# Optimization experiments

Hardware: AMD Instinct MI355X
Metric: run time of the kernel (lower is better)

## Reference

```python
import jax, jax.numpy as jnp
import numpy as np
from jax import lax

WS = (4, 8, 8)        # window_size (D,H,W)
DIM = 128
HEADS = 4
HD = DIM // HEADS      # 32
SCALE = HD ** -0.5     # swinv1, lif neuron -> head_dim**-0.5
TAU = 2.0
VTH = 1.0
ALPHA = 2.0            # ATan surrogate width


def _rel_pos_index(ws):
    # static numpy computation of relative_position_index, shape (N, N)
    coords = np.stack(np.meshgrid(np.arange(ws[0]), np.arange(ws[1]), np.arange(ws[2]), indexing='ij'))
    cf = coords.reshape(3, -1)                      # (3, N)
    rel = (cf[:, :, None] - cf[:, None, :]).transpose(1, 2, 0).astype(np.int64)  # (N,N,3)
    rel[:, :, 0] += ws[0] - 1
    rel[:, :, 1] += ws[1] - 1
    rel[:, :, 2] += ws[2] - 1
    rel[:, :, 0] *= (2 * ws[1] - 1) * (2 * ws[2] - 1)
    rel[:, :, 1] *= 2 * ws[2] - 1
    return rel.sum(-1)

RPI = _rel_pos_index(WS)  # (N, N) int


@jax.custom_vjp
def spike(x):
    return (x >= 0.0).astype(x.dtype)

def _spike_fwd(x):
    return spike(x), x

def _spike_bwd(x, g):
    # ATan surrogate gradient (spikingjelly default)
    return (g * (ALPHA / (2.0 * (1.0 + (np.pi / 2.0 * ALPHA * x) ** 2))),)

spike.defvjp(_spike_fwd, _spike_bwd)


def lif(x):
    # multi-step LIF over leading time axis: v' = v + (x - v)/tau, hard reset to 0
    def step(v, xt):
        v = v + (xt - v) / TAU
        s = spike(v - VTH)
        return v * (1.0 - s), s
    return lax.scan(step, jnp.zeros_like(x[0]), x)[1]


def setup_inputs() -> dict:
    key = jax.random.key(0)
    ks = jax.random.split(key, 7)
    x = jax.random.normal(ks[0], (WS[0], 256, WS[1], WS[2], DIM), dtype=jnp.float32)
    Wq = jax.random.normal(ks[1], (DIM, DIM), dtype=jnp.float32) * 0.02
    Wk = jax.random.normal(ks[2], (DIM, DIM), dtype=jnp.float32) * 0.02
    Wv = jax.random.normal(ks[3], (DIM, DIM), dtype=jnp.float32) * 0.02
    rpb_table = jax.random.normal(ks[4], ((2 * WS[0] - 1) * (2 * WS[1] - 1) * (2 * WS[2] - 1), HEADS), dtype=jnp.float32) * 0.02
    Wproj = jax.random.normal(ks[5], (DIM, DIM), dtype=jnp.float32) * 0.02
    bproj = jax.random.normal(ks[6], (DIM,), dtype=jnp.float32) * 0.02
    return {"x": x, "Wq": Wq, "Wk": Wk, "Wv": Wv, "rpb_table": rpb_table, "Wproj": Wproj, "bproj": bproj}


def reference(x, Wq, Wk, Wv, rpb_table, Wproj, bproj):
    T, B_, H, W, C = x.shape
    N = T * H * W
    # QKV: linear (no bias) -> spiking neuron over time axis
    q = lif(jnp.einsum('tbhwc,dc->tbhwd', x, Wq))
    k = lif(jnp.einsum('tbhwc,dc->tbhwd', x, Wk))
    v = lif(jnp.einsum('tbhwc,dc->tbhwd', x, Wv))
    # literal row-major reshape as in torch: (T,B_,H,W,C) -> (B_, heads, N, hd)
    q = q.reshape(B_, HEADS, N, HD)
    k = k.reshape(B_, HEADS, N, HD)
    v = v.reshape(B_, HEADS, N, HD)
    # scaled QK^T (NO softmax in the original forward)
    attn = jnp.einsum('bhnd,bhmd->bhnm', q * SCALE, k)
    rpb = rpb_table[RPI.reshape(-1)].reshape(N, N, HEADS).transpose(2, 0, 1)  # (heads,N,N)
    attn = attn + rpb[None]
    out = jnp.einsum('bhnm,bhmd->bhnd', attn, v)
    out = out.reshape(B_, HEADS, T, H, W, HD).transpose(2, 0, 3, 4, 1, 5).reshape(T, B_, H, W, C)
    out = jnp.einsum('tbhwc,dc->tbhwd', out, Wproj) + bproj
    out = lif(out).reshape(B_, N, C)
    return (out, attn)
```

## Files before the change

kernel.cpp:

```cpp
#include <hip/hip_runtime.h>
#include <hip/hip_bf16.h>


typedef __attribute__((ext_vector_type(8))) short bf16x8;
typedef __attribute__((ext_vector_type(4))) float f32x4;

#define MFMA16(a, b, c) __builtin_amdgcn_mfma_f32_16x16x32_bf16((a), (b), (c), 0, 0, 0)

__device__ __forceinline__ unsigned short f2bf(float f) {
    union { __hip_bfloat16 h; unsigned short u; } cv;
    cv.h = __float2bfloat16(f);
    return cv.u;
}
__device__ __forceinline__ float bf2f(unsigned short u) {
    union { unsigned int i; float f; } cv;
    cv.i = ((unsigned int)u) << 16;
    return cv.f;
}

__device__ __forceinline__ void cvt8_store(unsigned short* dst, const float* src) {
    float4 f0 = *(const float4*)(src);
    float4 f1 = *(const float4*)(src + 4);
    unsigned short h[8];
    h[0] = f2bf(f0.x); h[1] = f2bf(f0.y); h[2] = f2bf(f0.z); h[3] = f2bf(f0.w);
    h[4] = f2bf(f1.x); h[5] = f2bf(f1.y); h[6] = f2bf(f1.z); h[7] = f2bf(f1.w);
    *(uint4*)dst = *(const uint4*)h;
}

__global__ __launch_bounds__(256) void k_rpb_expand(
    const float* __restrict__ tbl, float* __restrict__ rpbx)
{
    int idx = blockIdx.x * 256 + threadIdx.x;
    int hh = idx >> 16;
    int n = (idx >> 8) & 255, m = idx & 255;
    int zn = n >> 6, yn = (n >> 3) & 7, xn = n & 7;
    int zm = m >> 6, ym = (m >> 3) & 7, xm = m & 7;
    int ri = (zn - zm + 3) * 225 + (yn - ym + 7) * 15 + (xn - xm + 7);
    rpbx[idx] = tbl[ri * 4 + hh];
}

__global__ __launch_bounds__(256) void k_qkv_lif(
    const float* __restrict__ x,
    const float* __restrict__ Wq,
    const float* __restrict__ Wk,
    const float* __restrict__ Wv,
    unsigned short* __restrict__ q_ws,
    unsigned short* __restrict__ k_ws,
    unsigned short* __restrict__ v_ws)
{
    __shared__ unsigned short Wl[128 * 136];
    __shared__ unsigned short Xl[64 * 136];

    const int tid = threadIdx.x;
    const int wv = tid >> 6, lane = tid & 63;
    const int l15 = lane & 15, lh = lane >> 4;
    const int wsel = blockIdx.y;
    const float* W = (wsel == 0) ? Wq : (wsel == 1) ? Wk : Wv;
    unsigned short* outp = (wsel == 0) ? q_ws : (wsel == 1) ? k_ws : v_ws;
    const int rowbase = blockIdx.x * 64;

    {
#pragma unroll
        for (int i = 0; i < 8; ++i) {
            int e = i * 2048 + tid * 8;
            int r = e >> 7, cc = e & 127;
            cvt8_store(&Wl[r * 136 + cc], W + r * 128 + cc);
        }
    }

    f32x4 vst[8];
#pragma unroll
    for (int nt = 0; nt < 8; ++nt) vst[nt] = (f32x4){0.f, 0.f, 0.f, 0.f};

    for (int t = 0; t < 4; ++t) {
        __syncthreads();
        const float* xg = x + t * 2097152 + rowbase * 128;
#pragma unroll
        for (int i = 0; i < 4; ++i) {
            int e = i * 2048 + tid * 8;
            int r = e >> 7, cc = e & 127;
            cvt8_store(&Xl[r * 136 + cc], xg + r * 128 + cc);
        }
        __syncthreads();

        f32x4 acc[8];
#pragma unroll
        for (int nt = 0; nt < 8; ++nt) acc[nt] = (f32x4){0.f, 0.f, 0.f, 0.f};
#pragma unroll
        for (int kk = 0; kk < 4; ++kk) {
            bf16x8 a = *(const bf16x8*)&Xl[(wv * 16 + l15) * 136 + kk * 32 + lh * 8];
#pragma unroll
            for (int nt = 0; nt < 8; ++nt) {
                bf16x8 b = *(const bf16x8*)&Wl[(nt * 16 + l15) * 136 + kk * 32 + lh * 8];
                acc[nt] = MFMA16(a, b, acc[nt]);
            }
        }
        unsigned short* og = outp + t * 2097152;
#pragma unroll
        for (int nt = 0; nt < 8; ++nt) {
#pragma unroll
            for (int reg = 0; reg < 4; ++reg) {
                float y = acc[nt][reg];
                float v = vst[nt][reg];
                v = v + (y - v) * 0.5f;
                float s = (v >= 1.0f) ? 1.0f : 0.0f;
                vst[nt][reg] = v * (1.0f - s);
                int r = rowbase + wv * 16 + lh * 4 + reg;
                og[r * 128 + nt * 16 + l15] =
                    (s != 0.0f) ? (unsigned short)0x3F80 : (unsigned short)0;
            }
        }
    }
}

__global__ __launch_bounds__(256) void k_attn(
    const unsigned short* __restrict__ q_ws,
    const unsigned short* __restrict__ k_ws,
    const unsigned short* __restrict__ v_ws,
    const float* __restrict__ rpbx,
    float* __restrict__ attn_out,
    unsigned short* __restrict__ o_ws)
{
    __shared__ unsigned int  qb[256];
    __shared__ unsigned short vT[32 * 264];
    __shared__ unsigned short attnL[64 * 264];

    const int tid = threadIdx.x;
    const int wv = tid >> 6, lane = tid & 63;
    const int l15 = lane & 15, lh = lane >> 4;
    const int hh = blockIdx.x & 3;
    const int base = blockIdx.x * 8192;

    {
        const unsigned short* qr = q_ws + base + tid * 32;
        unsigned int m = 0;
#pragma unroll
        for (int j = 0; j < 32; j += 8) {
            uint4 u = *(const uint4*)(qr + j);
            if (u.x & 0xFFFFu) m |= 1u << (j + 0);
            if (u.x >> 16)     m |= 1u << (j + 1);
            if (u.y & 0xFFFFu) m |= 1u << (j + 2);
            if (u.y >> 16)     m |= 1u << (j + 3);
            if (u.z & 0xFFFFu) m |= 1u << (j + 4);
            if (u.z >> 16)     m |= 1u << (j + 5);
            if (u.w & 0xFFFFu) m |= 1u << (j + 6);
            if (u.w >> 16)     m |= 1u << (j + 7);
        }
        qb[tid] = m;
    }
    unsigned int km = 0;
    {
        const unsigned short* kr = k_ws + base + tid * 32;
#pragma unroll
        for (int j = 0; j < 32; j += 8) {
            uint4 u = *(const uint4*)(kr + j);
            if (u.x & 0xFFFFu) km |= 1u << (j + 0);
            if (u.x >> 16)     km |= 1u << (j + 1);
            if (u.y & 0xFFFFu) km |= 1u << (j + 2);
            if (u.y >> 16)     km |= 1u << (j + 3);
            if (u.z & 0xFFFFu) km |= 1u << (j + 4);
            if (u.z >> 16)     km |= 1u << (j + 5);
            if (u.w & 0xFFFFu) km |= 1u << (j + 6);
            if (u.w >> 16)     km |= 1u << (j + 7);
        }
    }
    {
        const unsigned short* vr = v_ws + base + tid * 32;
#pragma unroll
        for (int j = 0; j < 32; j += 8) {
            uint4 u = *(const uint4*)(vr + j);
            vT[(j + 0) * 264 + tid] = (unsigned short)(u.x & 0xFFFFu);
            vT[(j + 1) * 264 + tid] = (unsigned short)(u.x >> 16);
            vT[(j + 2) * 264 + tid] = (unsigned short)(u.y & 0xFFFFu);
            vT[(j + 3) * 264 + tid] = (unsigned short)(u.y >> 16);
            vT[(j + 4) * 264 + tid] = (unsigned short)(u.z & 0xFFFFu);
            vT[(j + 5) * 264 + tid] = (unsigned short)(u.z >> 16);
            vT[(j + 6) * 264 + tid] = (unsigned short)(u.w & 0xFFFFu);
            vT[(j + 7) * 264 + tid] = (unsigned short)(u.w >> 16);
        }
    }
    __syncthreads();

    const float SC = 0.17677669529663687f;
    float* attn_b = attn_out + (size_t)blockIdx.x * 65536;
    const float* rp = rpbx + hh * 65536;
    unsigned short* ob = o_ws + base;

    for (int c = 0; c < 4; ++c) {
        for (int j = 0; j < 64; ++j) {
            int n = c * 64 + j;
            unsigned int qn = qb[n];
            int cnt = __popc(qn & km);
            float av = (float)cnt * SC + rp[n * 256 + tid];
            attnL[j * 264 + tid] = f2bf(av);
            attn_b[n * 256 + tid] = av;
        }
        __syncthreads();
        f32x4 oc[2];
        oc[0] = (f32x4){0.f, 0.f, 0.f, 0.f};
        oc[1] = (f32x4){0.f, 0.f, 0.f, 0.f};
#pragma unroll
        for (int kk = 0; kk < 8; ++kk) {
            bf16x8 a = *(const bf16x8*)&attnL[(wv * 16 + l15) * 264 + kk * 32 + lh * 8];
#pragma unroll
            for (int nt = 0; nt < 2; ++nt) {
                bf16x8 b = *(const bf16x8*)&vT[(nt * 16 + l15) * 264 + kk * 32 + lh * 8];
                oc[nt] = MFMA16(a, b, oc[nt]);
            }
        }
#pragma unroll
        for (int nt = 0; nt < 2; ++nt) {
#pragma unroll
            for (int reg = 0; reg < 4; ++reg) {
                int n = c * 64 + wv * 16 + lh * 4 + reg;
                ob[n * 32 + nt * 16 + l15] = f2bf(oc[nt][reg]);
            }
        }
        __syncthreads();
    }
}

__global__ __launch_bounds__(256) void k_proj_lif(
    const unsigned short* __restrict__ o_ws,
    const float* __restrict__ Wp,
    const float* __restrict__ bp,
    float* __restrict__ out0)
{
    __shared__ unsigned short Wl[128 * 136];
    __shared__ unsigned short Al[64 * 136];

    const int tid = threadIdx.x;
    const int wv = tid >> 6, lane = tid & 63;
    const int l15 = lane & 15, lh = lane >> 4;
    const int b = blockIdx.x;

    {
#pragma unroll
        for (int i = 0; i < 8; ++i) {
            int e = i * 2048 + tid * 8;
            int r = e >> 7, cc = e & 127;
            cvt8_store(&Wl[r * 136 + cc], Wp + r * 128 + cc);
        }
    }

    float biasf[2];
#pragma unroll
    for (int ntl = 0; ntl < 2; ++ntl)
        biasf[ntl] = bp[(wv * 2 + ntl) * 16 + l15];

    const unsigned short* ob = o_ws + b * 32768;

    for (int c = 0; c < 4; ++c) {
        __syncthreads();
#pragma unroll
        for (int i = 0; i < 4; ++i) {
            int e = i * 2048 + tid * 8;
            int lr2 = e >> 7, cc = e & 127;
            int t2 = lr2 >> 4, rit = lr2 & 15;
            int hhh = cc >> 5, hd = cc & 31;
            int n = t2 * 64 + c * 16 + rit;
            *(uint4*)&Al[lr2 * 136 + cc] =
                *(const uint4*)(ob + (hhh * 256 + n) * 32 + hd);
        }
        __syncthreads();

        f32x4 acc[4][2];
#pragma unroll
        for (int t2 = 0; t2 < 4; ++t2)
#pragma unroll
            for (int ntl = 0; ntl < 2; ++ntl)
                acc[t2][ntl] = (f32x4){0.f, 0.f, 0.f, 0.f};
#pragma unroll
        for (int kk = 0; kk < 4; ++kk) {
            bf16x8 a[4];
#pragma unroll
            for (int t2 = 0; t2 < 4; ++t2)
                a[t2] = *(const bf16x8*)&Al[(t2 * 16 + l15) * 136 + kk * 32 + lh * 8];
#pragma unroll
            for (int ntl = 0; ntl < 2; ++ntl) {
                bf16x8 bb = *(const bf16x8*)&Wl[((wv * 2 + ntl) * 16 + l15) * 136 + kk * 32 + lh * 8];
#pragma unroll
                for (int t2 = 0; t2 < 4; ++t2)
                    acc[t2][ntl] = MFMA16(a[t2], bb, acc[t2][ntl]);
            }
        }
#pragma unroll
        for (int ntl = 0; ntl < 2; ++ntl) {
            int d = (wv * 2 + ntl) * 16 + l15;
#pragma unroll
            for (int reg = 0; reg < 4; ++reg) {
                int hw = c * 16 + lh * 4 + reg;
                float v = 0.f;
#pragma unroll
                for (int t2 = 0; t2 < 4; ++t2) {
                    float y = acc[t2][ntl][reg] + biasf[ntl];
                    v = v + (y - v) * 0.5f;
                    float s = (v >= 1.0f) ? 1.0f : 0.0f;
                    v = v * (1.0f - s);
                    out0[t2 * 2097152 + b * 8192 + hw * 128 + d] = s;
                }
            }
        }
    }
}

extern "C" void kernel_launch(void* const* d_in, const int* in_sizes, int n_in,
                              void* d_out, int out_size, void* d_ws, size_t ws_size,
                              hipStream_t stream)
{
    const float* x   = (const float*)d_in[0];
    const float* Wq  = (const float*)d_in[1];
    const float* Wk  = (const float*)d_in[2];
    const float* Wv  = (const float*)d_in[3];
    const float* tbl = (const float*)d_in[4];
    const float* Wp  = (const float*)d_in[5];
    const float* bp  = (const float*)d_in[6];

    float* out0 = (float*)d_out;
    float* attn = out0 + 8388608;

    unsigned short* q_ws = (unsigned short*)d_ws;
    unsigned short* k_ws = q_ws + 8388608;
    unsigned short* v_ws = k_ws + 8388608;
    unsigned short* o_ws = v_ws + 8388608;
    float* rpbx = (float*)(o_ws + 8388608);

    k_rpb_expand<<<1024, 256, 0, stream>>>(tbl, rpbx);
    k_qkv_lif<<<dim3(256, 3), 256, 0, stream>>>(x, Wq, Wk, Wv, q_ws, k_ws, v_ws);
    k_attn<<<1024, 256, 0, stream>>>(q_ws, k_ws, v_ws, rpbx, attn, o_ws);
    k_proj_lif<<<256, 256, 0, stream>>>(o_ws, Wp, bp, out0);
}
```

Baseline: 380.1 us.

## Pack Q/K/V spikes into 32-bit bitmasks and vectorize attention score writes

The QKV LIF kernel now packs each 32-wide head row of binary spikes into one 32-bit mask through shared memory and writes that, instead of writing bf16 spike tensors. The attention kernel loads these masks directly and only expands V back to bf16 in LDS. This replaces roughly 48 MB of bf16 workspace traffic with about 3 MB. The attention score loop is also reorganized so each thread computes four columns with float4 bias loads and nontemporal float4 stores of the attention output. The cost is extra LDS round trips and barriers in the QKV kernel.

```diff
diff --git a/kernel.cpp b/kernel.cpp
--- a/kernel.cpp
+++ b/kernel.cpp
@@ -11,11 +11,6 @@
     union { __hip_bfloat16 h; unsigned short u; } cv;
     cv.h = __float2bfloat16(f);
     return cv.u;
-}
-__device__ __forceinline__ float bf2f(unsigned short u) {
-    union { unsigned int i; float f; } cv;
-    cv.i = ((unsigned int)u) << 16;
-    return cv.f;
 }
 
 __device__ __forceinline__ void cvt8_store(unsigned short* dst, const float* src) {
@@ -44,9 +39,9 @@
     const float* __restrict__ Wq,
     const float* __restrict__ Wk,
     const float* __restrict__ Wv,
-    unsigned short* __restrict__ q_ws,
-    unsigned short* __restrict__ k_ws,
-    unsigned short* __restrict__ v_ws)
+    unsigned int* __restrict__ qbits,
+    unsigned int* __restrict__ kbits,
+    unsigned int* __restrict__ vbits)
 {
     __shared__ unsigned short Wl[128 * 136];
     __shared__ unsigned short Xl[64 * 136];
@@ -56,8 +51,8 @@
     const int l15 = lane & 15, lh = lane >> 4;
     const int wsel = blockIdx.y;
     const float* W = (wsel == 0) ? Wq : (wsel == 1) ? Wk : Wv;
-    unsigned short* outp = (wsel == 0) ? q_ws : (wsel == 1) ? k_ws : v_ws;
-    const int rowbase = blockIdx.x * 64;
+    unsigned int* bits = (wsel == 0) ? qbits : (wsel == 1) ? kbits : vbits;
+    const int B = blockIdx.x;
 
     {
 #pragma unroll
@@ -74,7 +69,7 @@
 
     for (int t = 0; t < 4; ++t) {
         __syncthreads();
-        const float* xg = x + t * 2097152 + rowbase * 128;
+        const float* xg = x + t * 2097152 + B * 8192;
 #pragma unroll
         for (int i = 0; i < 4; ++i) {
             int e = i * 2048 + tid * 8;
@@ -95,7 +90,7 @@
                 acc[nt] = MFMA16(a, b, acc[nt]);
             }
         }
-        unsigned short* og = outp + t * 2097152;
+        unsigned short sp[8][4];
 #pragma unroll
         for (int nt = 0; nt < 8; ++nt) {
 #pragma unroll
@@ -105,18 +100,41 @@
                 v = v + (y - v) * 0.5f;
                 float s = (v >= 1.0f) ? 1.0f : 0.0f;
                 vst[nt][reg] = v * (1.0f - s);
-                int r = rowbase + wv * 16 + lh * 4 + reg;
-                og[r * 128 + nt * 16 + l15] =
-                    (s != 0.0f) ? (unsigned short)0x3F80 : (unsigned short)0;
-            }
+                sp[nt][reg] = (s != 0.0f) ? (unsigned short)1 : (unsigned short)0;
+            }
+        }
+        __syncthreads();
+#pragma unroll
+        for (int nt = 0; nt < 8; ++nt)
+#pragma unroll
+            for (int reg = 0; reg < 4; ++reg)
+                Xl[(wv * 16 + lh * 4 + reg) * 136 + nt * 16 + l15] = sp[nt][reg];
+        __syncthreads();
+        {
+            const unsigned short* rowp = &Xl[(tid >> 2) * 136 + (tid & 3) * 32];
+            unsigned int mask = 0;
+#pragma unroll
+            for (int j8 = 0; j8 < 4; ++j8) {
+                uint4 u = *(const uint4*)(rowp + j8 * 8);
+                int base = j8 * 8;
+                if (u.x & 0xFFFFu) mask |= 1u << (base + 0);
+                if (u.x >> 16)     mask |= 1u << (base + 1);
+                if (u.y & 0xFFFFu) mask |= 1u << (base + 2);
+                if (u.y >> 16)     mask |= 1u << (base + 3);
+                if (u.z & 0xFFFFu) mask |= 1u << (base + 4);
+                if (u.z >> 16)     mask |= 1u << (base + 5);
+                if (u.w & 0xFFFFu) mask |= 1u << (base + 6);
+                if (u.w >> 16)     mask |= 1u << (base + 7);
+            }
+            bits[(t * 256 + B) * 256 + tid] = mask;
         }
     }
 }
 
 __global__ __launch_bounds__(256) void k_attn(
-    const unsigned short* __restrict__ q_ws,
-    const unsigned short* __restrict__ k_ws,
-    const unsigned short* __restrict__ v_ws,
+    const unsigned int* __restrict__ qbits,
+    const unsigned int* __restrict__ kbits,
+    const unsigned int* __restrict__ vbits,
     const float* __restrict__ rpbx,
     float* __restrict__ attn_out,
     unsigned short* __restrict__ o_ws)
@@ -128,72 +146,41 @@
     const int tid = threadIdx.x;
     const int wv = tid >> 6, lane = tid & 63;
     const int l15 = lane & 15, lh = lane >> 4;
-    const int hh = blockIdx.x & 3;
-    const int base = blockIdx.x * 8192;
-
+    const int g = blockIdx.x, hh = g & 3;
+
+    qb[tid] = qbits[g * 256 + tid];
+    uint4 km = *(const uint4*)&kbits[g * 256 + (tid & 63) * 4];
     {
-        const unsigned short* qr = q_ws + base + tid * 32;
-        unsigned int m = 0;
-#pragma unroll
-        for (int j = 0; j < 32; j += 8) {
-            uint4 u = *(const uint4*)(qr + j);
-            if (u.x & 0xFFFFu) m |= 1u << (j + 0);
-            if (u.x >> 16)     m |= 1u << (j + 1);
-            if (u.y & 0xFFFFu) m |= 1u << (j + 2);
-            if (u.y >> 16)     m |= 1u << (j + 3);
-            if (u.z & 0xFFFFu) m |= 1u << (j + 4);
-            if (u.z >> 16)     m |= 1u << (j + 5);
-            if (u.w & 0xFFFFu) m |= 1u << (j + 6);
-            if (u.w >> 16)     m |= 1u << (j + 7);
-        }
-        qb[tid] = m;
-    }
-    unsigned int km = 0;
-    {
-        const unsigned short* kr = k_ws + base + tid * 32;
-#pragma unroll
-        for (int j = 0; j < 32; j += 8) {
-            uint4 u = *(const uint4*)(kr + j);
-            if (u.x & 0xFFFFu) km |= 1u << (j + 0);
-            if (u.x >> 16)     km |= 1u << (j + 1);
-            if (u.y & 0xFFFFu) km |= 1u << (j + 2);
-            if (u.y >> 16)     km |= 1u << (j + 3);
-            if (u.z & 0xFFFFu) km |= 1u << (j + 4);
-            if (u.z >> 16)     km |= 1u << (j + 5);
-            if (u.w & 0xFFFFu) km |= 1u << (j + 6);
-            if (u.w >> 16)     km |= 1u << (j + 7);
-        }
-    }
-    {
-        const unsigned short* vr = v_ws + base + tid * 32;
-#pragma unroll
-        for (int j = 0; j < 32; j += 8) {
-            uint4 u = *(const uint4*)(vr + j);
-            vT[(j + 0) * 264 + tid] = (unsigned short)(u.x & 0xFFFFu);
-            vT[(j + 1) * 264 + tid] = (unsigned short)(u.x >> 16);
-            vT[(j + 2) * 264 + tid] = (unsigned short)(u.y & 0xFFFFu);
-            vT[(j + 3) * 264 + tid] = (unsigned short)(u.y >> 16);
-            vT[(j + 4) * 264 + tid] = (unsigned short)(u.z & 0xFFFFu);
-            vT[(j + 5) * 264 + tid] = (unsigned short)(u.z >> 16);
-            vT[(j + 6) * 264 + tid] = (unsigned short)(u.w & 0xFFFFu);
-            vT[(j + 7) * 264 + tid] = (unsigned short)(u.w >> 16);
-        }
+        unsigned int vb = vbits[g * 256 + tid];
+#pragma unroll
+        for (int d = 0; d < 32; ++d)
+            vT[d * 264 + tid] = ((vb >> d) & 1u) ? (unsigned short)0x3F80
+                                                 : (unsigned short)0;
     }
     __syncthreads();
 
     const float SC = 0.17677669529663687f;
-    float* attn_b = attn_out + (size_t)blockIdx.x * 65536;
+    float* attn_b = attn_out + (size_t)g * 65536;
     const float* rp = rpbx + hh * 65536;
-    unsigned short* ob = o_ws + base;
+    unsigned short* ob = o_ws + g * 8192;
+    const int rg = tid >> 6, m0 = (tid & 63) * 4;
 
     for (int c = 0; c < 4; ++c) {
-        for (int j = 0; j < 64; ++j) {
-            int n = c * 64 + j;
+#pragma unroll
+        for (int j = 0; j < 16; ++j) {
+            int n = c * 64 + j * 4 + rg;
             unsigned int qn = qb[n];
-            int cnt = __popc(qn & km);
-            float av = (float)cnt * SC + rp[n * 256 + tid];
-            attnL[j * 264 + tid] = f2bf(av);
-            attn_b[n * 256 + tid] = av;
+            float4 rp4 = *(const float4*)&rp[n * 256 + m0];
+            f32x4 av;
+            av.x = (float)__popc(qn & km.x) * SC + rp4.x;
+            av.y = (float)__popc(qn & km.y) * SC + rp4.y;
+            av.z = (float)__popc(qn & km.z) * SC + rp4.z;
+            av.w = (float)__popc(qn & km.w) * SC + rp4.w;
+            __builtin_nontemporal_store(av, (f32x4*)(attn_b + n * 256 + m0));
+            unsigned int p0 = (unsigned int)f2bf(av.x) | ((unsigned int)f2bf(av.y) << 16);
+            unsigned int p1 = (unsigned int)f2bf(av.z) | ((unsigned int)f2bf(av.w) << 16);
+            uint2 pk; pk.x = p0; pk.y = p1;
+            *(uint2*)&attnL[(j * 4 + rg) * 264 + m0] = pk;
         }
         __syncthreads();
         f32x4 oc[2];
@@ -319,14 +306,14 @@
     float* out0 = (float*)d_out;
     float* attn = out0 + 8388608;
 
-    unsigned short* q_ws = (unsigned short*)d_ws;
-    unsigned short* k_ws = q_ws + 8388608;
-    unsigned short* v_ws = k_ws + 8388608;
-    unsigned short* o_ws = v_ws + 8388608;
-    float* rpbx = (float*)(o_ws + 8388608);
+    unsigned short* o_ws = (unsigned short*)d_ws;
+    unsigned int* qbits = (unsigned int*)(o_ws + 8388608);
+    unsigned int* kbits = qbits + 262144;
+    unsigned int* vbits = kbits + 262144;
+    float* rpbx = (float*)(vbits + 262144);
 
     k_rpb_expand<<<1024, 256, 0, stream>>>(tbl, rpbx);
-    k_qkv_lif<<<dim3(256, 3), 256, 0, stream>>>(x, Wq, Wk, Wv, q_ws, k_ws, v_ws);
-    k_attn<<<1024, 256, 0, stream>>>(q_ws, k_ws, v_ws, rpbx, attn, o_ws);
+    k_qkv_lif<<<dim3(256, 3), 256, 0, stream>>>(x, Wq, Wk, Wv, qbits, kbits, vbits);
+    k_attn<<<1024, 256, 0, stream>>>(qbits, kbits, vbits, rpbx, attn, o_ws);
     k_proj_lif<<<256, 256, 0, stream>>>(o_ws, Wp, bp, out0);
 }
```

Result: faster. 354.3 us (-6.8%).
